# Performance work log

Measured on AMD Instinct MI355X. Metric: run time of the kernel, lower is better.

## Reference

```python
import jax, jax.numpy as jnp
import numpy as np

BITS = 4
MAXQ = (1 << BITS) - 1  # 15
PACK = 32 // BITS       # 8 values per int32
GROUPSIZE = 128
IN_FEATURES = 4096
OUT_FEATURES = 11008
M_TOKENS = 4096


def setup_inputs() -> dict:
    key = jax.random.key(0)
    k1, k2, k3, k4, k5 = jax.random.split(key, 5)
    x = jax.random.normal(k1, (M_TOKENS, IN_FEATURES), dtype=jnp.float32)
    # packed 4-bit weights: [IN//8, OUT] int32, random bit patterns
    qweight = jax.random.randint(k2, (IN_FEATURES // PACK, OUT_FEATURES), 0, 2147483647, dtype=jnp.int32)
    n_groups = IN_FEATURES // GROUPSIZE  # 32
    scales = (jax.random.uniform(k3, (n_groups, OUT_FEATURES), dtype=jnp.float32) * 0.01 + 1e-4)
    qzeros = jax.random.randint(k4, (n_groups, OUT_FEATURES // PACK), 0, 2147483647, dtype=jnp.int32)
    g_idx = (jnp.arange(IN_FEATURES, dtype=jnp.int32) // GROUPSIZE).astype(jnp.int32)
    bias = jax.random.normal(k5, (OUT_FEATURES,), dtype=jnp.float32) * 0.01
    return {"x": x, "qweight": qweight, "scales": scales, "qzeros": qzeros, "g_idx": g_idx, "bias": bias}


def _dequantize(qweight, scales, qzeros, g_idx):
    """Unpack 4-bit fields and apply per-group scale/zero. Returns W [K, N] float."""
    shifts = (jnp.arange(PACK, dtype=jnp.int32) * BITS)
    # qweight [K//PACK, N] -> [K//PACK, PACK, N] -> [K, N]
    w = (qweight[:, None, :] >> shifts[None, :, None]) & MAXQ
    w = w.reshape(-1, qweight.shape[1])
    # qzeros [G, N//PACK] -> [G, N//PACK, PACK] -> [G, N]; kernel adds +1 (pack stored zeros-1)
    z = (qzeros[:, :, None] >> shifts[None, None, :]) & MAXQ
    z = z.reshape(qzeros.shape[0], -1) + 1
    # per-row group lookup via g_idx
    return scales[g_idx] * (w - z[g_idx]).astype(scales.dtype)


def reference(x, qweight, scales, qzeros, g_idx, bias):
    W = _dequantize(qweight, scales, qzeros, g_idx)  # [IN, OUT]
    out = jnp.matmul(x, W) + bias  # [M, OUT]
    return out
```

## Files before the change

### kernel.cpp

```cpp
#include <hip/hip_runtime.h>
#include <cstdint>
#include <cstddef>

typedef unsigned int u32;
typedef unsigned short u16;
typedef signed char s8;

typedef int i32x4 __attribute__((ext_vector_type(4)));
typedef u32 u32x2 __attribute__((ext_vector_type(2)));
typedef u32 u32x4 __attribute__((ext_vector_type(4)));
typedef float fvec4 __attribute__((ext_vector_type(4)));

#define M_DIM 4096
#define K_DIM 4096
#define N_DIM 11008

#define LDS_U32(p) ((__attribute__((address_space(3))) u32*)(uintptr_t)(p))
#define GLB_CU32(p) ((const __attribute__((address_space(1))) u32*)(uintptr_t)(p))

#if defined(__has_builtin)
#if __has_builtin(__builtin_amdgcn_mfma_i32_16x16x64_i8)
#define HAVE_MFMA_I8_BUILTIN 1
#endif
#endif

__device__ __forceinline__ i32x4 mfma_i8(i32x4 a, i32x4 b, i32x4 c) {
#ifdef HAVE_MFMA_I8_BUILTIN
    return __builtin_amdgcn_mfma_i32_16x16x64_i8(a, b, c, 0, 0, 0);
#else
    asm("v_mfma_i32_16x16x64_i8 %0, %1, %2, %0" : "+v"(c) : "v"(a), "v"(b));
    return c;
#endif
}

#define DQ_BLOCKS (172 * 32)
#define QT_BLOCKS M_DIM

__global__ __launch_bounds__(256) void prep_kernel(const float* __restrict__ x,
                                                   s8* __restrict__ x8,
                                                   float* __restrict__ alpha,
                                                   const int* __restrict__ qw,
                                                   const float* __restrict__ scales,
                                                   const int* __restrict__ qz,
                                                   float* __restrict__ Sn,
                                                   s8* __restrict__ wt) {
    __shared__ __align__(16) s8 sT[64][144];
    __shared__ float red[4][64];
    __shared__ float rcp[64];
    __shared__ float sm[4];

    const int tid = threadIdx.x;
    const int bx = blockIdx.x;

    if (bx >= DQ_BLOCKS) {
        const int row = bx - DQ_BLOCKS;
        const size_t base = (size_t)row * K_DIM + tid * 16;
        fvec4 v[4];
#pragma unroll
        for (int p = 0; p < 4; ++p)
            v[p] = __builtin_nontemporal_load((const fvec4*)(x + base + p * 4));
        float m = 0.f;
#pragma unroll
        for (int p = 0; p < 4; ++p)
#pragma unroll
            for (int e = 0; e < 4; ++e) m = fmaxf(m, fabsf(v[p][e]));
#pragma unroll
        for (int off = 32; off; off >>= 1) m = fmaxf(m, __shfl_xor(m, off));
        if ((tid & 63) == 0) sm[tid >> 6] = m;
        __syncthreads();
        m = fmaxf(fmaxf(sm[0], sm[1]), fmaxf(sm[2], sm[3]));
        const float inv = 127.f / m;
        if (tid == 0) alpha[row] = m * (1.f / 127.f);
        u32x4 o;
#pragma unroll
        for (int p = 0; p < 4; ++p) {
            u32 w = 0;
#pragma unroll
            for (int e = 0; e < 4; ++e) {
                const int q = (int)rintf(v[p][e] * inv);
                w |= ((u32)(q & 255)) << (8 * e);
            }
            o[p] = w;
        }
        *(u32x4*)(x8 + base) = o;
        return;
    }

    const int n0 = (bx % 172) * 64;
    const int g = bx / 172;
    const int n_sub = tid & 63;
    const int kc = tid >> 6;
    const int n = n0 + n_sub;

    float cmx = 0.f;
#pragma unroll
    for (int gg = 0; gg < 8; ++gg)
        cmx = fmaxf(cmx, scales[(size_t)(kc * 8 + gg) * N_DIM + n]);
    red[kc][n_sub] = cmx;
    __syncthreads();
    if (tid < 64) {
        const float m4 = fmaxf(fmaxf(red[0][tid], red[1][tid]),
                               fmaxf(red[2][tid], red[3][tid]));
        rcp[tid] = 127.f / (16.f * m4);
        if (g == 0) Sn[n0 + tid] = m4 * (16.f / 127.f);
    }
    __syncthreads();

    const float r = scales[(size_t)g * N_DIM + n] * rcp[n_sub];
    const int zq = __builtin_nontemporal_load(qz + (size_t)g * (N_DIM / 8) + (n >> 3));
    const int z = ((zq >> ((n & 7) * 4)) & 15) + 1;

#pragma unroll
    for (int j = 0; j < 4; ++j) {
        const int q = __builtin_nontemporal_load(qw + (size_t)(g * 16 + kc * 4 + j) * N_DIM + n);
        u32 lo = 0, hi = 0;
#pragma unroll
        for (int p = 0; p < 4; ++p) {
            const int v0 = (int)rintf((float)(((q >> (4 * p)) & 15) - z) * r);
            const int v1 = (int)rintf((float)(((q >> (4 * (p + 4))) & 15) - z) * r);
            lo |= ((u32)(v0 & 255)) << (8 * p);
            hi |= ((u32)(v1 & 255)) << (8 * p);
        }
        *(u32x2*)&sT[n_sub][kc * 32 + j * 8] = (u32x2){lo, hi};
    }

    __syncthreads();

    const int c = tid & 7;
    const int rr = tid >> 3;
#pragma unroll
    for (int it = 0; it < 2; ++it) {
        const int rw = it * 32 + rr;
        u32x4 v = *(const u32x4*)&sT[rw][c * 16];
        *(u32x4*)(wt + (size_t)(n0 + rw) * K_DIM + g * 128 + c * 16) = v;
    }
}

#define BAR() do { asm volatile("" ::: "memory"); __builtin_amdgcn_s_barrier(); asm volatile("" ::: "memory"); } while (0)
#define NT 32

__global__ __launch_bounds__(512, 2) void gemm_kernel(const s8* __restrict__ A,
                                                      const s8* __restrict__ B,
                                                      const float* __restrict__ alpha,
                                                      const float* __restrict__ Sn,
                                                      const float* __restrict__ bias,
                                                      float* __restrict__ C) {
    __shared__ __align__(16) s8 lds[131072];

    const int tid = threadIdx.x;
    const int wg = ((int)blockIdx.x & 7) * 86 + ((int)blockIdx.x >> 3);
    const int bm = (wg & 15) * 256;
    const int bn = (wg >> 4) * 256;

    const int lane = tid & 63;
    const int wv   = tid >> 6;
    const int wr   = wv >> 2;
    const int wc   = wv & 3;
    const int l16  = lane & 15;
    const int quad = lane >> 4;

    const int xr = tid >> 3;
    const int cc = (tid & 7) ^ (xr & 7);
    const s8* gs0 = A + (size_t)(bm + xr) * K_DIM + cc * 16;
    const s8* gs1 = A + (size_t)(bm + 64 + xr) * K_DIM + cc * 16;
    const s8* gs2 = B + (size_t)(bn + (xr >> 5) * 64 + (xr & 31)) * K_DIM + cc * 16;
    const s8* gs3 = B + (size_t)(bn + (xr >> 5) * 64 + 32 + (xr & 31)) * K_DIM + cc * 16;

#define ISSUE(r, bufsel, koff) do { \
    __builtin_amdgcn_global_load_lds(GLB_CU32(gs##r + (koff)), \
        LDS_U32(lds + (bufsel) * 65536 + (r) * 16384 + tid * 16), 16, 0, 0); \
    __builtin_amdgcn_global_load_lds(GLB_CU32(gs##r + (size_t)128 * K_DIM + (koff)), \
        LDS_U32(lds + (bufsel) * 65536 + (r) * 16384 + 8192 + tid * 16), 16, 0, 0); \
} while (0)

    const int kx = l16 & 7;
    const int cA = (quad ^ kx) * 16;
    const int tA = (wr * 64 + l16) * 128 + cA;
    const int tB = 32768 + (wc * 32 + l16) * 128 + cA;

    i32x4 acc[8][4];
#pragma unroll
    for (int i = 0; i < 8; ++i)
#pragma unroll
        for (int j = 0; j < 4; ++j) acc[i][j] = (i32x4){0, 0, 0, 0};

    ISSUE(0, 0, 0); ISSUE(2, 0, 0); ISSUE(3, 0, 0); ISSUE(1, 0, 0);
    ISSUE(0, 1, 128); ISSUE(2, 1, 128); ISSUE(3, 1, 128);
    asm volatile("s_waitcnt vmcnt(6)" ::: "memory");
    BAR();

    i32x4 af[4][2], b0f[2][2], b1f[2][2];

#pragma unroll
    for (int m = 0; m < 4; ++m) {
        const int o = tA + m * 2048;
        af[m][0] = *(const i32x4*)(lds + o);
        af[m][1] = *(const i32x4*)(lds + (o ^ 64));
    }
#pragma unroll
    for (int j = 0; j < 2; ++j) {
        const int o = tB + j * 2048;
        b0f[j][0] = *(const i32x4*)(lds + o);
        b0f[j][1] = *(const i32x4*)(lds + (o ^ 64));
        b1f[j][0] = *(const i32x4*)(lds + o + 16384);
        b1f[j][1] = *(const i32x4*)(lds + ((o ^ 64) + 16384));
    }

#pragma unroll 2
    for (int t = 0; t < NT; ++t) {
        const int buf = t & 1;
        const s8* sb = lds + buf * 65536;
        const s8* sn = lds + (buf ^ 1) * 65536;
        const bool pre = (t + 1 < NT);

        __builtin_amdgcn_s_setprio(1);
#pragma unroll
        for (int m = 0; m < 4; ++m) {
            acc[m][0] = mfma_i8(af[m][0], b0f[0][0], acc[m][0]);
            acc[m][0] = mfma_i8(af[m][1], b0f[0][1], acc[m][0]);
            acc[m][1] = mfma_i8(af[m][0], b0f[1][0], acc[m][1]);
            acc[m][1] = mfma_i8(af[m][1], b0f[1][1], acc[m][1]);
            acc[m][2] = mfma_i8(af[m][0], b1f[0][0], acc[m][2]);
            acc[m][2] = mfma_i8(af[m][1], b1f[0][1], acc[m][2]);
            acc[m][3] = mfma_i8(af[m][0], b1f[1][0], acc[m][3]);
            acc[m][3] = mfma_i8(af[m][1], b1f[1][1], acc[m][3]);
            const int o = tA + 16384 + m * 2048;
            af[m][0] = *(const i32x4*)(sb + o);
            af[m][1] = *(const i32x4*)(sb + (o ^ 64));
        }
        __builtin_amdgcn_s_setprio(0);
        if (pre) ISSUE(1, buf ^ 1, (t + 1) * 128);
        if (t < NT - 1) { asm volatile("s_waitcnt vmcnt(2)" ::: "memory"); }
        BAR();

        __builtin_amdgcn_s_setprio(1);
#pragma unroll
        for (int m = 0; m < 4; ++m) {
            acc[4 + m][0] = mfma_i8(af[m][0], b0f[0][0], acc[4 + m][0]);
            acc[4 + m][0] = mfma_i8(af[m][1], b0f[0][1], acc[4 + m][0]);
            acc[4 + m][1] = mfma_i8(af[m][0], b0f[1][0], acc[4 + m][1]);
            acc[4 + m][1] = mfma_i8(af[m][1], b0f[1][1], acc[4 + m][1]);
            acc[4 + m][2] = mfma_i8(af[m][0], b1f[0][0], acc[4 + m][2]);
            acc[4 + m][2] = mfma_i8(af[m][1], b1f[0][1], acc[4 + m][2]);
            acc[4 + m][3] = mfma_i8(af[m][0], b1f[1][0], acc[4 + m][3]);
            acc[4 + m][3] = mfma_i8(af[m][1], b1f[1][1], acc[4 + m][3]);
            if (pre) {
                const int o = tA + m * 2048;
                af[m][0] = *(const i32x4*)(sn + o);
                af[m][1] = *(const i32x4*)(sn + (o ^ 64));
            }
        }
        __builtin_amdgcn_s_setprio(0);
        if (pre) {
#pragma unroll
            for (int j = 0; j < 2; ++j) {
                const int o = tB + j * 2048;
                b0f[j][0] = *(const i32x4*)(sn + o);
                b0f[j][1] = *(const i32x4*)(sn + (o ^ 64));
                b1f[j][0] = *(const i32x4*)(sn + o + 16384);
                b1f[j][1] = *(const i32x4*)(sn + ((o ^ 64) + 16384));
            }
        }
        if (t + 2 < NT) { ISSUE(0, buf, (t + 2) * 128); ISSUE(2, buf, (t + 2) * 128); ISSUE(3, buf, (t + 2) * 128); }
        if (t < NT - 2)       { asm volatile("s_waitcnt vmcnt(6)" ::: "memory"); }
        else if (t == NT - 2) { asm volatile("s_waitcnt vmcnt(0)" ::: "memory"); }
        BAR();
    }
#undef ISSUE

    float sv[4], bv[4];
#pragma unroll
    for (int j = 0; j < 4; ++j) {
        const int col = bn + wc * 64 + j * 16 + l16;
        sv[j] = Sn[col];
        bv[j] = bias[col];
    }
#pragma unroll
    for (int i = 0; i < 8; ++i) {
#pragma unroll
        for (int r = 0; r < 4; ++r) {
            const int m = bm + wr * 128 + i * 16 + quad * 4 + r;
            const float am = alpha[m];
            float* cp = C + (size_t)m * N_DIM + bn + wc * 64 + l16;
#pragma unroll
            for (int j = 0; j < 4; ++j) {
                const float v = (float)acc[i][j][r] * (am * sv[j]) + bv[j];
                __builtin_nontemporal_store(v, cp + j * 16);
            }
        }
    }
}

__global__ __launch_bounds__(256) void fused_fallback(const float* __restrict__ x,
                                                      const int* __restrict__ qw,
                                                      const float* __restrict__ scales,
                                                      const int* __restrict__ qz,
                                                      const float* __restrict__ bias,
                                                      float* __restrict__ out) {
    __shared__ float sX[32 * 128];
    const int bm = blockIdx.y * 32;
    const int bn = blockIdx.x * 64;
    const int tid = threadIdx.x;
    const int nl = tid & 63;
    const int n = bn + nl;
    const int mg = tid >> 6;
    float acc[8] = {0, 0, 0, 0, 0, 0, 0, 0};

    for (int kt = 0; kt < K_DIM; kt += 128) {
        __syncthreads();
        for (int i = tid; i < 32 * 128; i += 256) {
            const int mm = i >> 7, kk = i & 127;
            sX[i] = x[(size_t)(bm + mm) * K_DIM + kt + kk];
        }
        __syncthreads();
        const int g = kt >> 7;
        const float scale = scales[(size_t)g * N_DIM + n];
        const int z = ((qz[(size_t)g * (N_DIM / 8) + (n >> 3)] >> ((n & 7) * 4)) & 15) + 1;
        for (int kp = 0; kp < 16; ++kp) {
            const int q = qw[(size_t)((kt >> 3) + kp) * N_DIM + n];
#pragma unroll
            for (int b = 0; b < 8; ++b) {
                const float w = scale * (float)(((q >> (4 * b)) & 15) - z);
                const int kk = kp * 8 + b;
#pragma unroll
                for (int mm = 0; mm < 8; ++mm)
                    acc[mm] += sX[(mg * 8 + mm) * 128 + kk] * w;
            }
        }
    }
#pragma unroll
    for (int mm = 0; mm < 8; ++mm)
        out[(size_t)(bm + mg * 8 + mm) * N_DIM + n] = acc[mm] + bias[n];
}

extern "C" void kernel_launch(void* const* d_in, const int* in_sizes, int n_in,
                              void* d_out, int out_size, void* d_ws, size_t ws_size,
                              hipStream_t stream) {
    const float* x      = (const float*)d_in[0];
    const int*   qw     = (const int*)d_in[1];
    const float* scales = (const float*)d_in[2];
    const int*   qz     = (const int*)d_in[3];
    const float* bias   = (const float*)d_in[5];
    float* out = (float*)d_out;

    const size_t x8_bytes = (size_t)M_DIM * K_DIM;
    const size_t wt_bytes = (size_t)N_DIM * K_DIM;
    const size_t al_bytes = (size_t)M_DIM * sizeof(float);
    const size_t sn_bytes = (size_t)N_DIM * sizeof(float);
    const size_t need = x8_bytes + wt_bytes + al_bytes + sn_bytes;

    if (ws_size >= need) {
        s8* x8     = (s8*)d_ws;
        s8* wt     = (s8*)d_ws + x8_bytes;
        float* al  = (float*)((char*)d_ws + x8_bytes + wt_bytes);
        float* Sn  = (float*)((char*)d_ws + x8_bytes + wt_bytes + al_bytes);
        prep_kernel<<<DQ_BLOCKS + QT_BLOCKS, 256, 0, stream>>>(x, x8, al, qw, scales, qz, Sn, wt);
        gemm_kernel<<<dim3((M_DIM / 256) * (N_DIM / 256)), dim3(512), 0, stream>>>(x8, wt, al, Sn, bias, out);
    } else {
        fused_fallback<<<dim3(N_DIM / 64, M_DIM / 32), 256, 0, stream>>>(x, qw, scales, qz, bias, out);
    }
}
```

Measured before the change: 422.9 us.

## Shrink GEMM block to 256x128 tile with four waves and restructured pipeline

The int8 MFMA GEMM moves from 512-thread blocks on 256x256 tiles to 256-thread blocks on 256x128 tiles. Each wave still computes a 128x64 output, and LDS drops to 96KB double-buffered. The K-loop is rewritten as two unrolled phases per step, with ping-pong B fragment registers, split async global-to-LDS issues (A0/B0 and then A1/B1), and explicit lgkmcnt/vmcnt waits. This aims for finer-grained overlap of loads with MFMA work and more blocks for load balance, at the cost of fewer waves per CU and more B-tile reloads across blocks.

```diff
diff --git a/kernel.cpp b/kernel.cpp
--- a/kernel.cpp
+++ b/kernel.cpp
@@ -139,44 +139,45 @@
 #define BAR() do { asm volatile("" ::: "memory"); __builtin_amdgcn_s_barrier(); asm volatile("" ::: "memory"); } while (0)
 #define NT 32
 
-__global__ __launch_bounds__(512, 2) void gemm_kernel(const s8* __restrict__ A,
+__global__ __launch_bounds__(256, 1) void gemm_kernel(const s8* __restrict__ A,
                                                       const s8* __restrict__ B,
                                                       const float* __restrict__ alpha,
                                                       const float* __restrict__ Sn,
                                                       const float* __restrict__ bias,
                                                       float* __restrict__ C) {
-    __shared__ __align__(16) s8 lds[131072];
+    __shared__ __align__(16) s8 lds[98304];
 
     const int tid = threadIdx.x;
-    const int wg = ((int)blockIdx.x & 7) * 86 + ((int)blockIdx.x >> 3);
+    const int wg = ((int)blockIdx.x & 7) * 172 + ((int)blockIdx.x >> 3);
     const int bm = (wg & 15) * 256;
-    const int bn = (wg >> 4) * 256;
+    const int bn = (wg >> 4) * 128;
 
     const int lane = tid & 63;
     const int wv   = tid >> 6;
-    const int wr   = wv >> 2;
-    const int wc   = wv & 3;
+    const int wr   = wv >> 1;
+    const int wc   = wv & 1;
     const int l16  = lane & 15;
     const int quad = lane >> 4;
 
     const int xr = tid >> 3;
     const int cc = (tid & 7) ^ (xr & 7);
-    const s8* gs0 = A + (size_t)(bm + xr) * K_DIM + cc * 16;
-    const s8* gs1 = A + (size_t)(bm + 64 + xr) * K_DIM + cc * 16;
-    const s8* gs2 = B + (size_t)(bn + (xr >> 5) * 64 + (xr & 31)) * K_DIM + cc * 16;
-    const s8* gs3 = B + (size_t)(bn + (xr >> 5) * 64 + 32 + (xr & 31)) * K_DIM + cc * 16;
-
-#define ISSUE(r, bufsel, koff) do { \
-    __builtin_amdgcn_global_load_lds(GLB_CU32(gs##r + (koff)), \
-        LDS_U32(lds + (bufsel) * 65536 + (r) * 16384 + tid * 16), 16, 0, 0); \
-    __builtin_amdgcn_global_load_lds(GLB_CU32(gs##r + (size_t)128 * K_DIM + (koff)), \
-        LDS_U32(lds + (bufsel) * 65536 + (r) * 16384 + 8192 + tid * 16), 16, 0, 0); \
-} while (0)
+    const s8* gsA = A + (size_t)(bm + xr) * K_DIM + cc * 16;
+    const s8* gsB = B + (size_t)(bn + xr) * K_DIM + cc * 16;
+
+#define IS1(gp, roff, koff, ldsoff) \
+    __builtin_amdgcn_global_load_lds(GLB_CU32((gp) + (size_t)(roff) * K_DIM + (koff)), \
+                                     LDS_U32(lds + (ldsoff) + tid * 16), 16, 0, 0)
+#define ISSUE_A0(bu, koff) do { IS1(gsA,   0, koff, (bu)*49152 +     0); IS1(gsA,  32, koff, (bu)*49152 +  4096); \
+                                IS1(gsA, 128, koff, (bu)*49152 +  8192); IS1(gsA, 160, koff, (bu)*49152 + 12288); } while (0)
+#define ISSUE_A1(bu, koff) do { IS1(gsA,  64, koff, (bu)*49152 + 16384); IS1(gsA,  96, koff, (bu)*49152 + 20480); \
+                                IS1(gsA, 192, koff, (bu)*49152 + 24576); IS1(gsA, 224, koff, (bu)*49152 + 28672); } while (0)
+#define ISSUE_B0(bu, koff) do { IS1(gsB,   0, koff, (bu)*49152 + 32768); IS1(gsB,  32, koff, (bu)*49152 + 36864); } while (0)
+#define ISSUE_B1(bu, koff) do { IS1(gsB,  64, koff, (bu)*49152 + 40960); IS1(gsB,  96, koff, (bu)*49152 + 45056); } while (0)
 
     const int kx = l16 & 7;
     const int cA = (quad ^ kx) * 16;
     const int tA = (wr * 64 + l16) * 128 + cA;
-    const int tB = 32768 + (wc * 32 + l16) * 128 + cA;
+    const int tB = 32768 + wc * 8192 + l16 * 128 + cA;
 
     i32x4 acc[8][4];
 #pragma unroll
@@ -184,89 +185,92 @@
 #pragma unroll
         for (int j = 0; j < 4; ++j) acc[i][j] = (i32x4){0, 0, 0, 0};
 
-    ISSUE(0, 0, 0); ISSUE(2, 0, 0); ISSUE(3, 0, 0); ISSUE(1, 0, 0);
-    ISSUE(0, 1, 128); ISSUE(2, 1, 128); ISSUE(3, 1, 128);
-    asm volatile("s_waitcnt vmcnt(6)" ::: "memory");
+    ISSUE_A0(0, 0); ISSUE_B0(0, 0); ISSUE_A1(0, 0); ISSUE_B1(0, 0);
+    ISSUE_A0(1, 128); ISSUE_B0(1, 128);
+    ISSUE_A1(1, 128); ISSUE_B1(1, 128);
+    asm volatile("s_waitcnt vmcnt(12)" ::: "memory");
     BAR();
 
-    i32x4 af[4][2], b0f[2][2], b1f[2][2];
+    i32x4 afLo[4][2], afHi[4][2], bE[4][2], bO[4][2];
 
 #pragma unroll
     for (int m = 0; m < 4; ++m) {
         const int o = tA + m * 2048;
-        af[m][0] = *(const i32x4*)(lds + o);
-        af[m][1] = *(const i32x4*)(lds + (o ^ 64));
-    }
-#pragma unroll
-    for (int j = 0; j < 2; ++j) {
+        afLo[m][0] = *(const i32x4*)(lds + o);
+        afLo[m][1] = *(const i32x4*)(lds + (o ^ 64));
+    }
+#pragma unroll
+    for (int j = 0; j < 4; ++j) {
         const int o = tB + j * 2048;
-        b0f[j][0] = *(const i32x4*)(lds + o);
-        b0f[j][1] = *(const i32x4*)(lds + (o ^ 64));
-        b1f[j][0] = *(const i32x4*)(lds + o + 16384);
-        b1f[j][1] = *(const i32x4*)(lds + ((o ^ 64) + 16384));
-    }
-
-#pragma unroll 2
-    for (int t = 0; t < NT; ++t) {
-        const int buf = t & 1;
-        const s8* sb = lds + buf * 65536;
-        const s8* sn = lds + (buf ^ 1) * 65536;
-        const bool pre = (t + 1 < NT);
-
-        __builtin_amdgcn_s_setprio(1);
-#pragma unroll
-        for (int m = 0; m < 4; ++m) {
-            acc[m][0] = mfma_i8(af[m][0], b0f[0][0], acc[m][0]);
-            acc[m][0] = mfma_i8(af[m][1], b0f[0][1], acc[m][0]);
-            acc[m][1] = mfma_i8(af[m][0], b0f[1][0], acc[m][1]);
-            acc[m][1] = mfma_i8(af[m][1], b0f[1][1], acc[m][1]);
-            acc[m][2] = mfma_i8(af[m][0], b1f[0][0], acc[m][2]);
-            acc[m][2] = mfma_i8(af[m][1], b1f[0][1], acc[m][2]);
-            acc[m][3] = mfma_i8(af[m][0], b1f[1][0], acc[m][3]);
-            acc[m][3] = mfma_i8(af[m][1], b1f[1][1], acc[m][3]);
-            const int o = tA + 16384 + m * 2048;
-            af[m][0] = *(const i32x4*)(sb + o);
-            af[m][1] = *(const i32x4*)(sb + (o ^ 64));
-        }
-        __builtin_amdgcn_s_setprio(0);
-        if (pre) ISSUE(1, buf ^ 1, (t + 1) * 128);
-        if (t < NT - 1) { asm volatile("s_waitcnt vmcnt(2)" ::: "memory"); }
-        BAR();
-
-        __builtin_amdgcn_s_setprio(1);
-#pragma unroll
-        for (int m = 0; m < 4; ++m) {
-            acc[4 + m][0] = mfma_i8(af[m][0], b0f[0][0], acc[4 + m][0]);
-            acc[4 + m][0] = mfma_i8(af[m][1], b0f[0][1], acc[4 + m][0]);
-            acc[4 + m][1] = mfma_i8(af[m][0], b0f[1][0], acc[4 + m][1]);
-            acc[4 + m][1] = mfma_i8(af[m][1], b0f[1][1], acc[4 + m][1]);
-            acc[4 + m][2] = mfma_i8(af[m][0], b1f[0][0], acc[4 + m][2]);
-            acc[4 + m][2] = mfma_i8(af[m][1], b1f[0][1], acc[4 + m][2]);
-            acc[4 + m][3] = mfma_i8(af[m][0], b1f[1][0], acc[4 + m][3]);
-            acc[4 + m][3] = mfma_i8(af[m][1], b1f[1][1], acc[4 + m][3]);
-            if (pre) {
-                const int o = tA + m * 2048;
-                af[m][0] = *(const i32x4*)(sn + o);
-                af[m][1] = *(const i32x4*)(sn + (o ^ 64));
-            }
-        }
-        __builtin_amdgcn_s_setprio(0);
-        if (pre) {
-#pragma unroll
-            for (int j = 0; j < 2; ++j) {
-                const int o = tB + j * 2048;
-                b0f[j][0] = *(const i32x4*)(sn + o);
-                b0f[j][1] = *(const i32x4*)(sn + (o ^ 64));
-                b1f[j][0] = *(const i32x4*)(sn + o + 16384);
-                b1f[j][1] = *(const i32x4*)(sn + ((o ^ 64) + 16384));
-            }
-        }
-        if (t + 2 < NT) { ISSUE(0, buf, (t + 2) * 128); ISSUE(2, buf, (t + 2) * 128); ISSUE(3, buf, (t + 2) * 128); }
-        if (t < NT - 2)       { asm volatile("s_waitcnt vmcnt(6)" ::: "memory"); }
-        else if (t == NT - 2) { asm volatile("s_waitcnt vmcnt(0)" ::: "memory"); }
-        BAR();
-    }
-#undef ISSUE
+        bE[j][0] = *(const i32x4*)(lds + o);
+        bE[j][1] = *(const i32x4*)(lds + (o ^ 64));
+    }
+
+#define TILE_PHASES(T, PAR, BCUR, BNXT) do {                                        \
+    const s8* sb = lds + (PAR) * 49152;                                             \
+    const s8* sn = lds + ((PAR) ^ 1) * 49152;                                       \
+    const bool pre1 = ((T) + 1 < NT);                                               \
+    const bool pre2 = ((T) + 2 < NT);                                               \
+      \
+    _Pragma("unroll")                                                               \
+    for (int m = 0; m < 4; ++m) {                                                   \
+        const int o = tA + 16384 + m * 2048;                                        \
+        afHi[m][0] = *(const i32x4*)(sb + o);                                       \
+        afHi[m][1] = *(const i32x4*)(sb + (o ^ 64));                                \
+    }                                                                               \
+    if (pre2) { ISSUE_A0((PAR), ((T) + 2) * 128); ISSUE_B0((PAR), ((T) + 2) * 128); } \
+    __builtin_amdgcn_s_setprio(1);                                                  \
+    _Pragma("unroll")                                                               \
+    for (int m = 0; m < 4; ++m)                                                     \
+        _Pragma("unroll")                                                           \
+        for (int j = 0; j < 4; ++j) {                                               \
+            acc[m][j] = mfma_i8(afLo[m][0], BCUR[j][0], acc[m][j]);                 \
+            acc[m][j] = mfma_i8(afLo[m][1], BCUR[j][1], acc[m][j]);                 \
+        }                                                                           \
+    __builtin_amdgcn_s_setprio(0);                                                  \
+    asm volatile("s_waitcnt lgkmcnt(0)" ::: "memory");                              \
+    if (pre2) { asm volatile("s_waitcnt vmcnt(6)" ::: "memory"); }                  \
+    else      { asm volatile("s_waitcnt vmcnt(0)" ::: "memory"); }                  \
+    BAR();                                                                          \
+      \
+    if (pre1) {                                                                     \
+        _Pragma("unroll")                                                           \
+        for (int m = 0; m < 4; ++m) {                                               \
+            const int o = tA + m * 2048;                                            \
+            afLo[m][0] = *(const i32x4*)(sn + o);                                   \
+            afLo[m][1] = *(const i32x4*)(sn + (o ^ 64));                            \
+        }                                                                           \
+        _Pragma("unroll")                                                           \
+        for (int j = 0; j < 4; ++j) {                                               \
+            const int o = tB + j * 2048;                                            \
+            BNXT[j][0] = *(const i32x4*)(sn + o);                                   \
+            BNXT[j][1] = *(const i32x4*)(sn + (o ^ 64));                            \
+        }                                                                           \
+    }                                                                               \
+    if (pre2) { ISSUE_A1((PAR), ((T) + 2) * 128); ISSUE_B1((PAR), ((T) + 2) * 128); } \
+    __builtin_amdgcn_s_setprio(1);                                                  \
+    _Pragma("unroll")                                                               \
+    for (int m = 0; m < 4; ++m)                                                     \
+        _Pragma("unroll")                                                           \
+        for (int j = 0; j < 4; ++j) {                                               \
+            acc[4 + m][j] = mfma_i8(afHi[m][0], BCUR[j][0], acc[4 + m][j]);         \
+            acc[4 + m][j] = mfma_i8(afHi[m][1], BCUR[j][1], acc[4 + m][j]);         \
+        }                                                                           \
+    __builtin_amdgcn_s_setprio(0);                                                  \
+    asm volatile("s_waitcnt lgkmcnt(0)" ::: "memory");                              \
+    BAR();                                                                          \
+} while (0)
+
+    for (int tp = 0; tp < NT; tp += 2) {
+        TILE_PHASES(tp,     0, bE, bO);
+        TILE_PHASES(tp + 1, 1, bO, bE);
+    }
+#undef TILE_PHASES
+#undef ISSUE_A0
+#undef ISSUE_A1
+#undef ISSUE_B0
+#undef ISSUE_B1
+#undef IS1
 
     float sv[4], bv[4];
 #pragma unroll
@@ -355,7 +359,7 @@
         float* al  = (float*)((char*)d_ws + x8_bytes + wt_bytes);
         float* Sn  = (float*)((char*)d_ws + x8_bytes + wt_bytes + al_bytes);
         prep_kernel<<<DQ_BLOCKS + QT_BLOCKS, 256, 0, stream>>>(x, x8, al, qw, scales, qz, Sn, wt);
-        gemm_kernel<<<dim3((M_DIM / 256) * (N_DIM / 256)), dim3(512), 0, stream>>>(x8, wt, al, Sn, bias, out);
+        gemm_kernel<<<dim3((M_DIM / 256) * (N_DIM / 128)), dim3(256), 0, stream>>>(x8, wt, al, Sn, bias, out);
     } else {
         fused_fallback<<<dim3(N_DIM / 64, M_DIM / 32), 256, 0, stream>>>(x, qw, scales, qz, bias, out);
     }
```

New measurement: 459.5 us. 1.09x slower.
